# Kernel tuning notes

Measured on AMD Instinct MI355X. Metric: run time of the kernel, lower is better.

The kernel has to match this reference:

```python
import jax, jax.numpy as jnp
import numpy as np

B, S, DIM, SDIM = 4, 4096, 1024, 256


def setup_inputs() -> dict:
    key = jax.random.key(0)
    ks = jax.random.split(key, 10)
    def lin(k, din, dout):
        return jax.random.normal(k, (din, dout), jnp.float32) / np.float32(np.sqrt(din))
    return {
        "x": jax.random.normal(ks[0], (B, S, DIM), jnp.float32),
        "ln_g": jnp.ones((DIM,), jnp.float32),
        "ln_b": jnp.zeros((DIM,), jnp.float32),
        "mix_w": jax.random.normal(ks[1], (DIM, 1, 3), jnp.float32) * 0.3,  # depthwise conv kernel
        "mix_b": jnp.zeros((DIM,), jnp.float32),
        "Wi": lin(ks[2], DIM, DIM), "bi": jnp.zeros((DIM,), jnp.float32),
        "Wsin": lin(ks[3], DIM, SDIM), "bsin": jnp.zeros((SDIM,), jnp.float32),
        "Wd": lin(ks[4], DIM, SDIM), "bd": jnp.zeros((SDIM,), jnp.float32),
        "Wsel": lin(ks[5], DIM, SDIM), "bsel": jnp.zeros((SDIM,), jnp.float32),
        "Wso": lin(ks[6], SDIM, DIM), "bso": jnp.zeros((DIM,), jnp.float32),
        "Wg": lin(ks[7], DIM, DIM), "bg": jnp.zeros((DIM,), jnp.float32),
        "Wout": lin(ks[8], DIM, DIM), "bout": jnp.zeros((DIM,), jnp.float32),
    }


def reference(x, ln_g, ln_b, mix_w, mix_b, Wi, bi, Wsin, bsin, Wd, bd,
              Wsel, bsel, Wso, bso, Wg, bg, Wout, bout):
    eps = 1e-5
    # LayerNorm over last dim
    mu = jnp.mean(x, axis=-1, keepdims=True)
    var = jnp.mean(jnp.square(x - mu), axis=-1, keepdims=True)
    h = (x - mu) * jax.lax.rsqrt(var + eps) * ln_g + ln_b
    # depthwise Conv1d, kernel=3, padding=1, groups=dim
    hc = jnp.transpose(h, (0, 2, 1))  # [B, C, L]
    mixed = jax.lax.conv_general_dilated(
        hc, mix_w, window_strides=(1,), padding=[(1, 1)],
        dimension_numbers=("NCH", "OIH", "NCH"), feature_group_count=hc.shape[1])
    mixed = jnp.transpose(mixed + mix_b[None, :, None], (0, 2, 1))  # [B, S, D]
    u = jnp.tanh(mixed @ Wi + bi)                 # [B, S, D]
    x_state = jnp.tanh(mixed @ Wsin + bsin)       # [B, S, N]
    decay = jax.nn.sigmoid(mixed @ Wd + bd)       # [B, S, N]
    select = jax.nn.sigmoid(mixed @ Wsel + bsel)  # [B, S, N]
    # sequential linear recurrence: state = d*state + (1-d)*x_state
    def step(state, inp):
        dt, xt = inp
        state = dt * state + (1.0 - dt) * xt
        return state, state
    init = jnp.zeros((x.shape[0], x_state.shape[-1]), x.dtype)
    _, states = jax.lax.scan(step, init,
                             (jnp.swapaxes(decay, 0, 1), jnp.swapaxes(x_state, 0, 1)))
    states = jnp.swapaxes(states, 0, 1)           # [B, S, N]
    y = (select * states) @ Wso + bso             # [B, S, D]
    g = jax.nn.sigmoid(mixed @ Wg + bg)
    out = (g * y + (1.0 - g) * u) @ Wout + bout
    return x + out
```

## Files before the change

kernel.cpp:

```cpp
#include <hip/hip_runtime.h>
#include <hip/hip_bf16.h>
#include <math.h>

typedef __bf16 bf16_t;
typedef __bf16 bf16x8 __attribute__((ext_vector_type(8)));
typedef __bf16 bf16x4 __attribute__((ext_vector_type(4)));
typedef float  f32x4  __attribute__((ext_vector_type(4)));

#define B_ 4
#define S_ 4096
#define D_ 1024
#define N_ 256
#define M_ (B_*S_)

__device__ __forceinline__ float fsig(float x){
    return __builtin_amdgcn_rcpf(1.0f + __expf(-x));
}
__device__ __forceinline__ float ftanh(float x){
    return 1.0f - 2.0f*__builtin_amdgcn_rcpf(1.0f + __expf(2.0f*x));
}

struct TJobs {
    const float* in[7];
    bf16_t*      out[7];
    int R[7];
    int C[7];
};

__global__ void transpose_all(TJobs j){
    int z = blockIdx.z;
    int R = j.R[z], C = j.C[z];
    int c0 = blockIdx.x*32, r0 = blockIdx.y*32;
    if (c0 >= C || r0 >= R) return;
    __shared__ float tile[32][33];
    int tx = threadIdx.x, ty = threadIdx.y;
    const float* in = j.in[z];
    bf16_t* out = j.out[z];
    #pragma unroll
    for (int i=0;i<32;i+=8)
        tile[ty+i][tx] = in[(size_t)(r0+ty+i)*C + (c0+tx)];
    __syncthreads();
    #pragma unroll
    for (int i=0;i<32;i+=8)
        out[(size_t)(c0+ty+i)*R + (r0+tx)] = (bf16_t)tile[tx][ty+i];
}

__global__ void ln_kernel(const float* __restrict__ x, const float* __restrict__ gw,
                          const float* __restrict__ bw, bf16_t* __restrict__ h){
    int row = blockIdx.x;
    int t = threadIdx.x;
    float4 v = ((const float4*)(x + (size_t)row*D_))[t];
    float s = v.x+v.y+v.z+v.w;
    float q = v.x*v.x+v.y*v.y+v.z*v.z+v.w*v.w;
    #pragma unroll
    for (int o=1;o<64;o<<=1){ s += __shfl_xor(s,o,64); q += __shfl_xor(q,o,64); }
    __shared__ float sw[4], sq[4];
    int wid = t>>6;
    if ((t&63)==0){ sw[wid]=s; sq[wid]=q; }
    __syncthreads();
    s = sw[0]+sw[1]+sw[2]+sw[3];
    q = sq[0]+sq[1]+sq[2]+sq[3];
    float mu = s*(1.0f/D_);
    float rs = rsqrtf(q*(1.0f/D_) - mu*mu + 1e-5f);
    float4 gv = ((const float4*)gw)[t];
    float4 bv = ((const float4*)bw)[t];
    bf16x4 o4;
    o4[0] = (bf16_t)((v.x-mu)*rs*gv.x + bv.x);
    o4[1] = (bf16_t)((v.y-mu)*rs*gv.y + bv.y);
    o4[2] = (bf16_t)((v.z-mu)*rs*gv.z + bv.z);
    o4[3] = (bf16_t)((v.w-mu)*rs*gv.w + bv.w);
    *(bf16x4*)(h + (size_t)row*D_ + t*4) = o4;
}

__global__ void conv_kernel(const bf16_t* __restrict__ h, const float* __restrict__ w,
                            const float* __restrict__ mb, bf16_t* __restrict__ mix){
    int idx = blockIdx.x*256 + threadIdx.x;
    int g8  = idx & 127;
    int row = idx >> 7;
    int s   = row & (S_-1);
    int d0  = g8*8;
    const bf16_t* hr = h + (size_t)row*D_ + d0;
    bf16x8 cur = *(const bf16x8*)hr;
    bf16x8 prv, nxt;
    #pragma unroll
    for (int i=0;i<8;i++){ prv[i]=(bf16_t)0.0f; nxt[i]=(bf16_t)0.0f; }
    if (s > 0)      prv = *(const bf16x8*)(hr - D_);
    if (s < S_-1)   nxt = *(const bf16x8*)(hr + D_);
    bf16x8 ov;
    #pragma unroll
    for (int i=0;i<8;i++){
        int d = d0+i;
        float o = (float)prv[i]*w[d*3] + (float)cur[i]*w[d*3+1] + (float)nxt[i]*w[d*3+2] + mb[d];
        ov[i] = (bf16_t)o;
    }
    *(bf16x8*)(mix + (size_t)row*D_ + d0) = ov;
}

struct Epi {
    const float *b0,*b1,*b2,*b3,*b4;
    bf16_t *u, *g, *z;
    bf16_t *xs, *dc, *sel;
    const bf16_t *gbuf, *ubuf;
    const float *resid;
    float *outp;
};

#define LDSW 40

template<int MODE>
__global__ __launch_bounds__(256,3)
void gemm_kernel(const bf16_t* __restrict__ A, const bf16_t* __restrict__ Bt,
                 int K, Epi e){
    __shared__ __align__(16) char smem[40960];
    bf16_t* As = (bf16_t*)smem;
    bf16_t* Bs = (bf16_t*)(smem + 20480);
    const int BUF = 128*LDSW;
    int tid  = threadIdx.x;
    int m0   = blockIdx.x*128;
    int n0   = blockIdx.y*128;
    int wave = tid>>6, lane = tid&63;
    int wm = (wave>>1)*64, wn = (wave&1)*64;
    int lm = lane&15, quad = lane>>4;

    f32x4 acc[4][4];
    #pragma unroll
    for (int i=0;i<4;i++)
        #pragma unroll
        for (int j=0;j<4;j++)
            #pragma unroll
            for (int r=0;r<4;r++) acc[i][j][r]=0.0f;

    int ar = tid>>2;
    int ac = (tid&3)*8;
    const bf16_t* pA0 = A  + (size_t)(m0+ar   )*K + ac;
    const bf16_t* pA1 = A  + (size_t)(m0+ar+64)*K + ac;
    const bf16_t* pB0 = Bt + (size_t)(n0+ar   )*K + ac;
    const bf16_t* pB1 = Bt + (size_t)(n0+ar+64)*K + ac;
    int w0 = (ar   )*LDSW + ac;
    int w1 = (ar+64)*LDSW + ac;

    int aOff[4], bOff[4];
    #pragma unroll
    for (int i=0;i<4;i++){
        aOff[i] = (wm+i*16+lm)*LDSW + quad*8;
        bOff[i] = (wn+i*16+lm)*LDSW + quad*8;
    }

    bf16x8 ra0 = *(const bf16x8*)(pA0);
    bf16x8 ra1 = *(const bf16x8*)(pA1);
    bf16x8 rb0 = *(const bf16x8*)(pB0);
    bf16x8 rb1 = *(const bf16x8*)(pB1);
    *(bf16x8*)&As[w0] = ra0;
    *(bf16x8*)&As[w1] = ra1;
    *(bf16x8*)&Bs[w0] = rb0;
    *(bf16x8*)&Bs[w1] = rb1;
    if (K > 32){
        ra0 = *(const bf16x8*)(pA0 + 32);
        ra1 = *(const bf16x8*)(pA1 + 32);
        rb0 = *(const bf16x8*)(pB0 + 32);
        rb1 = *(const bf16x8*)(pB1 + 32);
    }

    int buf = 0;
    for (int k0=0; k0<K; k0+=32, buf^=1){
        __syncthreads();
        int nb = (buf^1)*BUF;
        if (k0+32 < K){
            *(bf16x8*)&As[nb+w0] = ra0;
            *(bf16x8*)&As[nb+w1] = ra1;
            *(bf16x8*)&Bs[nb+w0] = rb0;
            *(bf16x8*)&Bs[nb+w1] = rb1;
            if (k0+64 < K){
                ra0 = *(const bf16x8*)(pA0 + k0+64);
                ra1 = *(const bf16x8*)(pA1 + k0+64);
                rb0 = *(const bf16x8*)(pB0 + k0+64);
                rb1 = *(const bf16x8*)(pB1 + k0+64);
            }
        }
        int cb = buf*BUF;
        bf16x8 aF[4], bF[4];
        #pragma unroll
        for (int i=0;i<4;i++){
            aF[i] = *(const bf16x8*)&As[cb+aOff[i]];
            bF[i] = *(const bf16x8*)&Bs[cb+bOff[i]];
        }
        #pragma unroll
        for (int i=0;i<4;i++)
            #pragma unroll
            for (int j=0;j<4;j++)
                acc[i][j] = __builtin_amdgcn_mfma_f32_16x16x32_bf16(aF[i], bF[j], acc[i][j], 0,0,0);
    }

    if (MODE==2){
        float* T = (float*)smem;
        #pragma unroll
        for (int p=0;p<2;p++){
            __syncthreads();
            if (wn == p*64){
                #pragma unroll
                for (int i=0;i<4;i++)
                    #pragma unroll
                    for (int j=0;j<4;j++)
                        #pragma unroll
                        for (int r=0;r<4;r++)
                            T[(wm+i*16+quad*4+r)*68 + j*16+lm] = acc[i][j][r];
            }
            __syncthreads();
            int c4 = tid&15;
            int gcol = n0 + p*64 + c4*4;
            float4 bias = *(const float4*)&e.b0[gcol];
            #pragma unroll
            for (int it=0; it<8; it++){
                int rr = (tid>>4) + it*16;
                f32x4 v = *(const f32x4*)&T[rr*68 + c4*4];
                size_t gi = (size_t)(m0+rr)*D_ + gcol;
                float4 res = *(const float4*)&e.resid[gi];
                float4 o;
                o.x = v[0]+res.x+bias.x; o.y = v[1]+res.y+bias.y;
                o.z = v[2]+res.z+bias.z; o.w = v[3]+res.w+bias.w;
                *(float4*)&e.outp[gi] = o;
            }
        }
    } else {
        bf16_t* Tb = (bf16_t*)smem;
        __syncthreads();
        if (MODE==0){
            const float* bp; int cbase; bool ut = (n0 < 1280);
            if (n0 < 1024){ bp=e.b0; cbase=n0; }
            else if (n0 < 1792){
                int sub=(n0-1024)>>8;
                bp = sub==0? e.b1 : sub==1? e.b2 : e.b3;
                cbase = (n0-1024)&255;
            } else { bp=e.b4; cbase=n0-1792; }
            #pragma unroll
            for (int i=0;i<4;i++)
                #pragma unroll
                for (int j=0;j<4;j++){
                    float bv = bp[cbase + wn+j*16+lm];
                    #pragma unroll
                    for (int r=0;r<4;r++){
                        float v = acc[i][j][r] + bv;
                        v = ut ? ftanh(v) : fsig(v);
                        Tb[(wm+i*16+quad*4+r)*136 + wn+j*16+lm] = (bf16_t)v;
                    }
                }
        } else {
            #pragma unroll
            for (int i=0;i<4;i++)
                #pragma unroll
                for (int j=0;j<4;j++){
                    float bv = e.b0[n0 + wn+j*16+lm];
                    #pragma unroll
                    for (int r=0;r<4;r++)
                        Tb[(wm+i*16+quad*4+r)*136 + wn+j*16+lm] = (bf16_t)(acc[i][j][r] + bv);
                }
        }
        __syncthreads();
        int ch = tid&15;
        if (MODE==0){
            bf16_t* dst; int width, colbase;
            if (n0 < 1024){ dst=e.u; width=D_; colbase=n0; }
            else if (n0 < 1792){
                int sub=(n0-1024)>>8;
                dst = sub==0? e.xs : sub==1? e.dc : e.sel;
                width=N_; colbase=(n0-1024)&255;
            } else { dst=e.g; width=D_; colbase=n0-1792; }
            #pragma unroll
            for (int it=0; it<8; it++){
                int rr = (tid>>4) + it*16;
                bf16x8 v = *(const bf16x8*)&Tb[rr*136 + ch*8];
                *(bf16x8*)&dst[(size_t)(m0+rr)*width + colbase + ch*8] = v;
            }
        } else {
            #pragma unroll
            for (int it=0; it<8; it++){
                int rr = (tid>>4) + it*16;
                bf16x8 y = *(const bf16x8*)&Tb[rr*136 + ch*8];
                size_t gi = (size_t)(m0+rr)*D_ + n0 + ch*8;
                bf16x8 gv = *(const bf16x8*)&e.gbuf[gi];
                bf16x8 uv = *(const bf16x8*)&e.ubuf[gi];
                bf16x8 o;
                #pragma unroll
                for (int q=0;q<8;q++){
                    float gf = (float)gv[q];
                    o[q] = (bf16_t)(gf*(float)y[q] + (1.0f-gf)*(float)uv[q]);
                }
                *(bf16x8*)&e.z[gi] = o;
            }
        }
    }
}

__global__ void scan_p1(const bf16_t* __restrict__ dc, const bf16_t* __restrict__ xs,
                        float* __restrict__ aggA, float* __restrict__ aggB){
    int bc = blockIdx.x;
    int b = bc>>6, ch = bc&63;
    int n = threadIdx.x;
    size_t base = ((size_t)b*S_ + ch*64)*N_ + n;
    float A = 1.0f, Bc = 0.0f;
    for (int t=0;t<64;t++){
        float d = (float)dc[base + (size_t)t*N_];
        float x = (float)xs[base + (size_t)t*N_];
        A  = d*A;
        Bc = d*Bc + (1.0f-d)*x;
    }
    aggA[(size_t)bc*N_+n]=A; aggB[(size_t)bc*N_+n]=Bc;
}

__global__ void scan_p2(const float* __restrict__ aggA, const float* __restrict__ aggB,
                        float* __restrict__ pre){
    int b = blockIdx.x, n = threadIdx.x;
    float s = 0.0f;
    for (int ch=0; ch<64; ch++){
        size_t i = ((size_t)b*64+ch)*N_+n;
        pre[i] = s;
        s = aggA[i]*s + aggB[i];
    }
}

__global__ void scan_p3(const bf16_t* __restrict__ dc, const bf16_t* __restrict__ xs,
                        const bf16_t* __restrict__ sel, const float* __restrict__ pre,
                        bf16_t* __restrict__ ss){
    int bc = blockIdx.x;
    int b = bc>>6, ch = bc&63;
    int n = threadIdx.x;
    size_t base = ((size_t)b*S_ + ch*64)*N_ + n;
    float s = pre[(size_t)bc*N_+n];
    for (int t=0;t<64;t++){
        size_t i = base + (size_t)t*N_;
        float d = (float)dc[i], x = (float)xs[i];
        s = d*s + (1.0f-d)*x;
        ss[i] = (bf16_t)((float)sel[i]*s);
    }
}

extern "C" void kernel_launch(void* const* d_in, const int* in_sizes, int n_in,
                              void* d_out, int out_size, void* d_ws, size_t ws_size,
                              hipStream_t stream){
    const float* x    = (const float*)d_in[0];
    const float* ln_g = (const float*)d_in[1];
    const float* ln_b = (const float*)d_in[2];
    const float* mixw = (const float*)d_in[3];
    const float* mixb = (const float*)d_in[4];
    const float* Wi   = (const float*)d_in[5];
    const float* bi   = (const float*)d_in[6];
    const float* Wsin = (const float*)d_in[7];
    const float* bsin = (const float*)d_in[8];
    const float* Wd   = (const float*)d_in[9];
    const float* bd   = (const float*)d_in[10];
    const float* Wsel = (const float*)d_in[11];
    const float* bsel = (const float*)d_in[12];
    const float* Wso  = (const float*)d_in[13];
    const float* bso  = (const float*)d_in[14];
    const float* Wg   = (const float*)d_in[15];
    const float* bg   = (const float*)d_in[16];
    const float* Wout = (const float*)d_in[17];
    const float* bout = (const float*)d_in[18];
    float* out = (float*)d_out;

    char* p = (char*)d_ws;
    auto alloc = [&](size_t bytes)->char*{ char* r=p; p += (bytes+255)&~(size_t)255; return r; };
    bf16_t* hB    = (bf16_t*)alloc((size_t)M_*D_*2);
    bf16_t* mixB  = (bf16_t*)alloc((size_t)M_*D_*2);
    bf16_t* uB    = (bf16_t*)alloc((size_t)M_*D_*2);
    bf16_t* gB    = (bf16_t*)alloc((size_t)M_*D_*2);
    bf16_t* ssB   = (bf16_t*)alloc((size_t)M_*N_*2);
    bf16_t* xs    = (bf16_t*)alloc((size_t)M_*N_*2);
    bf16_t* dc    = (bf16_t*)alloc((size_t)M_*N_*2);
    bf16_t* sel   = (bf16_t*)alloc((size_t)M_*N_*2);
    bf16_t* WbigT = (bf16_t*)alloc((size_t)2816*1024*2);
    bf16_t* WsoT  = (bf16_t*)alloc(1024*256*2);
    bf16_t* WoutT = (bf16_t*)alloc(1024*1024*2);
    float*  aggA  = (float*)alloc((size_t)4*64*256*4);
    float*  aggB  = (float*)alloc((size_t)4*64*256*4);
    float*  pre   = (float*)alloc((size_t)4*64*256*4);
    bf16_t* zB = mixB;

    TJobs tj;
    tj.in[0]=Wi;   tj.out[0]=WbigT;            tj.R[0]=1024; tj.C[0]=1024;
    tj.in[1]=Wsin; tj.out[1]=WbigT+1024*1024;  tj.R[1]=1024; tj.C[1]=256;
    tj.in[2]=Wd;   tj.out[2]=WbigT+1280*1024;  tj.R[2]=1024; tj.C[2]=256;
    tj.in[3]=Wsel; tj.out[3]=WbigT+1536*1024;  tj.R[3]=1024; tj.C[3]=256;
    tj.in[4]=Wg;   tj.out[4]=WbigT+(size_t)1792*1024; tj.R[4]=1024; tj.C[4]=1024;
    tj.in[5]=Wso;  tj.out[5]=WsoT;             tj.R[5]=256;  tj.C[5]=1024;
    tj.in[6]=Wout; tj.out[6]=WoutT;            tj.R[6]=1024; tj.C[6]=1024;
    transpose_all<<<dim3(32,32,7), dim3(32,8), 0, stream>>>(tj);

    ln_kernel  <<<M_, 256, 0, stream>>>(x, ln_g, ln_b, hB);
    conv_kernel<<<M_*128/256, 256, 0, stream>>>(hB, mixw, mixb, mixB);

    Epi e0 = {};
    e0.b0=bi; e0.b1=bsin; e0.b2=bd; e0.b3=bsel; e0.b4=bg;
    e0.u=uB; e0.g=gB; e0.xs=xs; e0.dc=dc; e0.sel=sel;
    gemm_kernel<0><<<dim3(M_/128, 22), 256, 0, stream>>>(mixB, WbigT, 1024, e0);

    scan_p1<<<4*64, 256, 0, stream>>>(dc, xs, aggA, aggB);
    scan_p2<<<4,    256, 0, stream>>>(aggA, aggB, pre);
    scan_p3<<<4*64, 256, 0, stream>>>(dc, xs, sel, pre, ssB);

    Epi e1 = {};
    e1.b0=bso; e1.gbuf=gB; e1.ubuf=uB; e1.z=zB;
    gemm_kernel<1><<<dim3(M_/128, 8), 256, 0, stream>>>(ssB, WsoT, 256, e1);

    Epi e2 = {};
    e2.b0=bout; e2.resid=x; e2.outp=out;
    gemm_kernel<2><<<dim3(M_/128, 8), 256, 0, stream>>>(zB, WoutT, 1024, e2);
}
```

Measured before the change: 401.8 us.

## Replace GEMM with 256x256 tiles using direct global-to-LDS loads

Rewrites the shared GEMM kernel to use 256x256 output tiles with 512 threads (8 waves, each computing 128x64). Operand tiles are loaded with global_load_lds straight into double-buffered LDS, with explicit vmcnt waits, barriers and MFMA priority raising. The larger tiles raise arithmetic intensity and remove the register round trip of the old staging. In exchange it uses more registers per wave, fewer blocks (lower occupancy and wave-tail risk), and an unpadded LDS layout that may cause bank conflicts.

```diff
diff --git a/kernel.cpp b/kernel.cpp
--- a/kernel.cpp
+++ b/kernel.cpp
@@ -18,6 +18,12 @@
 }
 __device__ __forceinline__ float ftanh(float x){
     return 1.0f - 2.0f*__builtin_amdgcn_rcpf(1.0f + __expf(2.0f*x));
+}
+
+__device__ __forceinline__ void gload_lds16(const void* g, void* l){
+    __builtin_amdgcn_global_load_lds(
+        (const __attribute__((address_space(1))) unsigned int*)g,
+        (__attribute__((address_space(3))) unsigned int*)l, 16, 0, 0);
 }
 
 struct TJobs {
@@ -105,187 +111,200 @@
     float *outp;
 };
 
-#define LDSW 40
+#define WAITV4() asm volatile("s_waitcnt vmcnt(4)" ::: "memory")
+#define WAITV0() asm volatile("s_waitcnt vmcnt(0)" ::: "memory")
+#define CFENCE() asm volatile("" ::: "memory")
+#define BARR()   __builtin_amdgcn_s_barrier()
 
 template<int MODE>
-__global__ __launch_bounds__(256,3)
-void gemm_kernel(const bf16_t* __restrict__ A, const bf16_t* __restrict__ Bt,
-                 int K, Epi e){
-    __shared__ __align__(16) char smem[40960];
-    bf16_t* As = (bf16_t*)smem;
-    bf16_t* Bs = (bf16_t*)(smem + 20480);
-    const int BUF = 128*LDSW;
-    int tid  = threadIdx.x;
-    int m0   = blockIdx.x*128;
-    int n0   = blockIdx.y*128;
-    int wave = tid>>6, lane = tid&63;
-    int wm = (wave>>1)*64, wn = (wave&1)*64;
+__global__ __launch_bounds__(512,2)
+void gemm256(const bf16_t* __restrict__ A, const bf16_t* __restrict__ Bt,
+             int K, Epi e){
+    extern __shared__ __align__(16) char lds[];
+    const int TILE = 16384;
+    int t = threadIdx.x;
+    int wave = t>>6, lane = t&63;
+    int wm = (wave>>2)*128;
+    int wn = (wave&3)*64;
     int lm = lane&15, quad = lane>>4;
-
-    f32x4 acc[4][4];
-    #pragma unroll
-    for (int i=0;i<4;i++)
+    int m0 = blockIdx.x*256, n0 = blockIdx.y*256;
+    int NT = K>>5;
+
+    int srow = t>>2;
+    int scol = (t&3)*8;
+    const bf16_t* gA = A  + (size_t)(m0+srow)*K + scol;
+    const bf16_t* gB = Bt + (size_t)(n0+srow)*K + scol;
+
+    auto stage = [&](int kt, int buf){
+        const bf16_t* a = gA + kt*32;
+        const bf16_t* b = gB + kt*32;
+        char* da = lds + buf*TILE + t*16;
+        char* db = lds + 32768 + buf*TILE + t*16;
+        gload_lds16(a,                  da);
+        gload_lds16(a + (size_t)128*K,  da + 8192);
+        gload_lds16(b,                  db);
+        gload_lds16(b + (size_t)128*K,  db + 8192);
+    };
+
+    int raBase = (wm+lm)*64 + quad*16;
+    int rbBase = (wn+lm)*64 + quad*16;
+
+    f32x4 acc[8][4];
+    #pragma unroll
+    for (int i=0;i<8;i++)
         #pragma unroll
         for (int j=0;j<4;j++)
             #pragma unroll
             for (int r=0;r<4;r++) acc[i][j][r]=0.0f;
 
-    int ar = tid>>2;
-    int ac = (tid&3)*8;
-    const bf16_t* pA0 = A  + (size_t)(m0+ar   )*K + ac;
-    const bf16_t* pA1 = A  + (size_t)(m0+ar+64)*K + ac;
-    const bf16_t* pB0 = Bt + (size_t)(n0+ar   )*K + ac;
-    const bf16_t* pB1 = Bt + (size_t)(n0+ar+64)*K + ac;
-    int w0 = (ar   )*LDSW + ac;
-    int w1 = (ar+64)*LDSW + ac;
-
-    int aOff[4], bOff[4];
-    #pragma unroll
-    for (int i=0;i<4;i++){
-        aOff[i] = (wm+i*16+lm)*LDSW + quad*8;
-        bOff[i] = (wn+i*16+lm)*LDSW + quad*8;
-    }
-
-    bf16x8 ra0 = *(const bf16x8*)(pA0);
-    bf16x8 ra1 = *(const bf16x8*)(pA1);
-    bf16x8 rb0 = *(const bf16x8*)(pB0);
-    bf16x8 rb1 = *(const bf16x8*)(pB1);
-    *(bf16x8*)&As[w0] = ra0;
-    *(bf16x8*)&As[w1] = ra1;
-    *(bf16x8*)&Bs[w0] = rb0;
-    *(bf16x8*)&Bs[w1] = rb1;
-    if (K > 32){
-        ra0 = *(const bf16x8*)(pA0 + 32);
-        ra1 = *(const bf16x8*)(pA1 + 32);
-        rb0 = *(const bf16x8*)(pB0 + 32);
-        rb1 = *(const bf16x8*)(pB1 + 32);
-    }
-
-    int buf = 0;
-    for (int k0=0; k0<K; k0+=32, buf^=1){
-        __syncthreads();
-        int nb = (buf^1)*BUF;
-        if (k0+32 < K){
-            *(bf16x8*)&As[nb+w0] = ra0;
-            *(bf16x8*)&As[nb+w1] = ra1;
-            *(bf16x8*)&Bs[nb+w0] = rb0;
-            *(bf16x8*)&Bs[nb+w1] = rb1;
-            if (k0+64 < K){
-                ra0 = *(const bf16x8*)(pA0 + k0+64);
-                ra1 = *(const bf16x8*)(pA1 + k0+64);
-                rb0 = *(const bf16x8*)(pB0 + k0+64);
-                rb1 = *(const bf16x8*)(pB1 + k0+64);
-            }
-        }
-        int cb = buf*BUF;
-        bf16x8 aF[4], bF[4];
-        #pragma unroll
-        for (int i=0;i<4;i++){
-            aF[i] = *(const bf16x8*)&As[cb+aOff[i]];
-            bF[i] = *(const bf16x8*)&Bs[cb+bOff[i]];
-        }
+    bf16x8 aF[8], bF[4];
+
+    stage(0,0);
+    stage(1,1);
+    WAITV4();
+    BARR();
+
+    for (int kt=0; kt<NT; ++kt){
+        int buf = kt&1;
+        const char* pa = lds + buf*TILE + raBase;
+        const char* pb = lds + 32768 + buf*TILE + rbBase;
+
+        #pragma unroll
+        for (int i=0;i<4;i++) aF[i] = *(const bf16x8*)(pa + i*1024);
+        #pragma unroll
+        for (int j=0;j<4;j++) bF[j] = *(const bf16x8*)(pb + j*1024);
+        BARR();
+        asm volatile("s_waitcnt lgkmcnt(0)" ::: "memory");
+        __builtin_amdgcn_sched_barrier(0);
+        __builtin_amdgcn_s_setprio(1);
         #pragma unroll
         for (int i=0;i<4;i++)
             #pragma unroll
             for (int j=0;j<4;j++)
                 acc[i][j] = __builtin_amdgcn_mfma_f32_16x16x32_bf16(aF[i], bF[j], acc[i][j], 0,0,0);
-    }
-
-    if (MODE==2){
-        float* T = (float*)smem;
-        #pragma unroll
-        for (int p=0;p<2;p++){
+        __builtin_amdgcn_s_setprio(0);
+        __builtin_amdgcn_sched_barrier(0);
+        BARR();
+
+        #pragma unroll
+        for (int i=0;i<4;i++) aF[4+i] = *(const bf16x8*)(pa + (4+i)*1024);
+        BARR();
+        asm volatile("s_waitcnt lgkmcnt(0)" ::: "memory");
+        __builtin_amdgcn_sched_barrier(0);
+        __builtin_amdgcn_s_setprio(1);
+        #pragma unroll
+        for (int i=0;i<4;i++)
+            #pragma unroll
+            for (int j=0;j<4;j++)
+                acc[4+i][j] = __builtin_amdgcn_mfma_f32_16x16x32_bf16(aF[4+i], bF[j], acc[4+i][j], 0,0,0);
+        __builtin_amdgcn_s_setprio(0);
+        __builtin_amdgcn_sched_barrier(0);
+        BARR();
+
+        if (kt+2 < NT){
+            CFENCE();
+            stage(kt+2, buf);
+            WAITV4();
+            BARR();
+        } else if (kt+1 < NT){
+            WAITV0();
+            BARR();
+        }
+    }
+    __syncthreads();
+
+    if (MODE==0 || MODE==1){
+        const float* bp = e.b0; int cbase = 0; bf16_t* dst = 0; int width = D_;
+        bool ut = true;
+        if (MODE==0){
+            ut = (n0 < 1280);
+            if (n0 < 1024){ bp=e.b0; cbase=n0; dst=e.u; width=D_; }
+            else if (n0 < 1792){
+                int sub=(n0-1024)>>8;
+                bp  = sub==0? e.b1 : sub==1? e.b2 : e.b3;
+                dst = sub==0? e.xs : sub==1? e.dc : e.sel;
+                cbase = 0; width = N_;
+            } else { bp=e.b4; cbase=n0-1792; dst=e.g; width=D_; }
+        } else {
+            bp = e.b0; cbase = n0; width = D_;
+        }
+        bf16_t* Tb = (bf16_t*)lds;
+        #pragma unroll
+        for (int h=0; h<4; h++){
+            if (h) __syncthreads();
+            if (wm == (h>>1)*128){
+                int ib = (h&1)*4;
+                #pragma unroll
+                for (int ii=0;ii<4;ii++){
+                    #pragma unroll
+                    for (int j=0;j<4;j++){
+                        float bv = bp[(MODE==0?cbase:n0) + wn + j*16 + lm];
+                        #pragma unroll
+                        for (int r=0;r<4;r++){
+                            float v = acc[ib+ii][j][r] + bv;
+                            if (MODE==0) v = ut ? ftanh(v) : fsig(v);
+                            Tb[(ii*16+quad*4+r)*264 + wn + j*16 + lm] = (bf16_t)v;
+                        }
+                    }
+                }
+            }
             __syncthreads();
-            if (wn == p*64){
+            if (MODE==0){
                 #pragma unroll
-                for (int i=0;i<4;i++)
+                for (int it=0; it<4; it++){
+                    int idx = it*512 + t;
+                    int row = idx>>5, c8 = idx&31;
+                    bf16x8 v = *(const bf16x8*)&Tb[row*264 + c8*8];
+                    *(bf16x8*)&dst[(size_t)(m0 + h*64 + row)*width + cbase + c8*8] = v;
+                }
+            } else {
+                #pragma unroll
+                for (int it=0; it<4; it++){
+                    int idx = it*512 + t;
+                    int row = idx>>5, c8 = idx&31;
+                    bf16x8 y = *(const bf16x8*)&Tb[row*264 + c8*8];
+                    size_t gi = (size_t)(m0 + h*64 + row)*D_ + n0 + c8*8;
+                    bf16x8 gv = *(const bf16x8*)&e.gbuf[gi];
+                    bf16x8 uv = *(const bf16x8*)&e.ubuf[gi];
+                    bf16x8 o;
+                    #pragma unroll
+                    for (int q=0;q<8;q++){
+                        float gf = (float)gv[q];
+                        o[q] = (bf16_t)(gf*(float)y[q] + (1.0f-gf)*(float)uv[q]);
+                    }
+                    *(bf16x8*)&e.z[gi] = o;
+                }
+            }
+        }
+    } else {
+        float* T = (float*)lds;
+        #pragma unroll
+        for (int pZ=0; pZ<8; pZ++){
+            if (pZ) __syncthreads();
+            if (wm == (pZ>>2)*128){
+                int ib = (pZ&3)*2;
+                #pragma unroll
+                for (int ii=0;ii<2;ii++){
                     #pragma unroll
                     for (int j=0;j<4;j++)
                         #pragma unroll
                         for (int r=0;r<4;r++)
-                            T[(wm+i*16+quad*4+r)*68 + j*16+lm] = acc[i][j][r];
+                            T[(ii*16+quad*4+r)*260 + wn + j*16 + lm] = acc[ib+ii][j][r];
+                }
             }
             __syncthreads();
-            int c4 = tid&15;
-            int gcol = n0 + p*64 + c4*4;
-            float4 bias = *(const float4*)&e.b0[gcol];
             #pragma unroll
-            for (int it=0; it<8; it++){
-                int rr = (tid>>4) + it*16;
-                f32x4 v = *(const f32x4*)&T[rr*68 + c4*4];
-                size_t gi = (size_t)(m0+rr)*D_ + gcol;
+            for (int it=0; it<4; it++){
+                int idx = it*512 + t;
+                int row = idx>>6, c4 = idx&63;
+                f32x4 v = *(const f32x4*)&T[row*260 + c4*4];
+                size_t gi = (size_t)(m0 + pZ*32 + row)*D_ + n0 + c4*4;
                 float4 res = *(const float4*)&e.resid[gi];
+                float4 bb  = *(const float4*)&e.b0[n0 + c4*4];
                 float4 o;
-                o.x = v[0]+res.x+bias.x; o.y = v[1]+res.y+bias.y;
-                o.z = v[2]+res.z+bias.z; o.w = v[3]+res.w+bias.w;
+                o.x = v[0]+res.x+bb.x; o.y = v[1]+res.y+bb.y;
+                o.z = v[2]+res.z+bb.z; o.w = v[3]+res.w+bb.w;
                 *(float4*)&e.outp[gi] = o;
-            }
-        }
-    } else {
-        bf16_t* Tb = (bf16_t*)smem;
-        __syncthreads();
-        if (MODE==0){
-            const float* bp; int cbase; bool ut = (n0 < 1280);
-            if (n0 < 1024){ bp=e.b0; cbase=n0; }
-            else if (n0 < 1792){
-                int sub=(n0-1024)>>8;
-                bp = sub==0? e.b1 : sub==1? e.b2 : e.b3;
-                cbase = (n0-1024)&255;
-            } else { bp=e.b4; cbase=n0-1792; }
-            #pragma unroll
-            for (int i=0;i<4;i++)
-                #pragma unroll
-                for (int j=0;j<4;j++){
-                    float bv = bp[cbase + wn+j*16+lm];
-                    #pragma unroll
-                    for (int r=0;r<4;r++){
-                        float v = acc[i][j][r] + bv;
-                        v = ut ? ftanh(v) : fsig(v);
-                        Tb[(wm+i*16+quad*4+r)*136 + wn+j*16+lm] = (bf16_t)v;
-                    }
-                }
-        } else {
-            #pragma unroll
-            for (int i=0;i<4;i++)
-                #pragma unroll
-                for (int j=0;j<4;j++){
-                    float bv = e.b0[n0 + wn+j*16+lm];
-                    #pragma unroll
-                    for (int r=0;r<4;r++)
-                        Tb[(wm+i*16+quad*4+r)*136 + wn+j*16+lm] = (bf16_t)(acc[i][j][r] + bv);
-                }
-        }
-        __syncthreads();
-        int ch = tid&15;
-        if (MODE==0){
-            bf16_t* dst; int width, colbase;
-            if (n0 < 1024){ dst=e.u; width=D_; colbase=n0; }
-            else if (n0 < 1792){
-                int sub=(n0-1024)>>8;
-                dst = sub==0? e.xs : sub==1? e.dc : e.sel;
-                width=N_; colbase=(n0-1024)&255;
-            } else { dst=e.g; width=D_; colbase=n0-1792; }
-            #pragma unroll
-            for (int it=0; it<8; it++){
-                int rr = (tid>>4) + it*16;
-                bf16x8 v = *(const bf16x8*)&Tb[rr*136 + ch*8];
-                *(bf16x8*)&dst[(size_t)(m0+rr)*width + colbase + ch*8] = v;
-            }
-        } else {
-            #pragma unroll
-            for (int it=0; it<8; it++){
-                int rr = (tid>>4) + it*16;
-                bf16x8 y = *(const bf16x8*)&Tb[rr*136 + ch*8];
-                size_t gi = (size_t)(m0+rr)*D_ + n0 + ch*8;
-                bf16x8 gv = *(const bf16x8*)&e.gbuf[gi];
-                bf16x8 uv = *(const bf16x8*)&e.ubuf[gi];
-                bf16x8 o;
-                #pragma unroll
-                for (int q=0;q<8;q++){
-                    float gf = (float)gv[q];
-                    o[q] = (bf16_t)(gf*(float)y[q] + (1.0f-gf)*(float)uv[q]);
-                }
-                *(bf16x8*)&e.z[gi] = o;
             }
         }
     }
@@ -392,7 +411,7 @@
     Epi e0 = {};
     e0.b0=bi; e0.b1=bsin; e0.b2=bd; e0.b3=bsel; e0.b4=bg;
     e0.u=uB; e0.g=gB; e0.xs=xs; e0.dc=dc; e0.sel=sel;
-    gemm_kernel<0><<<dim3(M_/128, 22), 256, 0, stream>>>(mixB, WbigT, 1024, e0);
+    gemm256<0><<<dim3(M_/256, 11), 512, 65536, stream>>>(mixB, WbigT, 1024, e0);
 
     scan_p1<<<4*64, 256, 0, stream>>>(dc, xs, aggA, aggB);
     scan_p2<<<4,    256, 0, stream>>>(aggA, aggB, pre);
@@ -400,9 +419,9 @@
 
     Epi e1 = {};
     e1.b0=bso; e1.gbuf=gB; e1.ubuf=uB; e1.z=zB;
-    gemm_kernel<1><<<dim3(M_/128, 8), 256, 0, stream>>>(ssB, WsoT, 256, e1);
+    gemm256<1><<<dim3(M_/256, 4), 512, 65536, stream>>>(ssB, WsoT, 256, e1);
 
     Epi e2 = {};
     e2.b0=bout; e2.resid=x; e2.outp=out;
-    gemm_kernel<2><<<dim3(M_/128, 8), 256, 0, stream>>>(zB, WoutT, 1024, e2);
-}
+    gemm256<2><<<dim3(M_/256, 4), 512, 65536, stream>>>(zB, WoutT, 1024, e2);
+}
```

Measured after the change: 429.8 us. 7.0% more time.
